# Optimization experiments

Measured on AMD Instinct MI355X. Metric: run time of the kernel, lower is better.

Reference implementation:

```python
import jax, jax.numpy as jnp
import numpy as np

B, N, DIM = 4, 4096, 512
HEADS, DIM_HEAD = 8, 64
DIM_INNER = HEADS * DIM_HEAD


def setup_inputs() -> dict:
    key = jax.random.key(0)
    k1, k2, k3 = jax.random.split(key, 3)
    x = jax.random.normal(k1, (B, N, DIM), dtype=jnp.float32)
    mask = jax.random.bernoulli(k2, 0.9, (B, N))
    W_qkv = jax.random.normal(k3, (DIM, 3 * DIM_INNER), dtype=jnp.float32) * (1.0 / np.sqrt(DIM))
    b_qkv = jnp.zeros((3 * DIM_INNER,), dtype=jnp.float32)
    return {"x": x, "mask": mask, "W_qkv": W_qkv, "b_qkv": b_qkv}


def reference(x, mask, W_qkv, b_qkv):
    # qkv projection: [b, n, 3*h*d]
    qkv = jnp.einsum('bnc,ce->bne', x, W_qkv) + b_qkv
    q, k, v = jnp.split(qkv, 3, axis=-1)

    def to_heads(t):  # b n (h d) -> b h n d
        b, n, _ = t.shape
        return t.reshape(b, n, HEADS, DIM_HEAD).transpose(0, 2, 1, 3)

    q, k, v = map(to_heads, (q, k, v))

    m = mask[:, None, :, None]  # b 1 n 1
    neg_max = -jnp.finfo(q.dtype).max
    k = jnp.where(m, k, neg_max)
    v = jnp.where(m, v, 0.0)

    k = jax.nn.softmax(k, axis=-2)  # softmax over sequence
    q = jax.nn.softmax(q, axis=-1)  # softmax over feature dim

    kv = jnp.einsum('bhnd,bhne->bhde', k, v)   # [b, h, d, d]
    out = jnp.einsum('bhde,bhnd->bhne', kv, q)  # [b, h, n, d]
    b_, h_, n_, d_ = out.shape
    return out.transpose(0, 2, 1, 3).reshape(b_, n_, h_ * d_)
```

## Files before the change

kernel.cpp:

```cpp
#include <hip/hip_runtime.h>
#include <stdint.h>

#define B_   4
#define N_   4096
#define DIM_ 512
#define H_   8
#define DH_  64
#define E3_  1536
#define M_   (B_*N_)

typedef __attribute__((ext_vector_type(8))) __bf16 bf16x8;
typedef __attribute__((ext_vector_type(8))) unsigned short ushort8;
typedef __attribute__((ext_vector_type(4))) float f32x4;

__device__ inline float bf2f(unsigned short u){ return __uint_as_float(((unsigned)u)<<16); }
__device__ inline unsigned short f2bf(float f){
  unsigned u = __float_as_uint(f);
  u += 0x7FFFu + ((u>>16)&1u);
  return (unsigned short)(u>>16);
}

__device__ inline void gld_lds16(const void* g, void* l){
  __builtin_amdgcn_global_load_lds(
      (const __attribute__((address_space(1))) void*)g,
      (__attribute__((address_space(3))) void*)l, 16, 0, 0);
}

__global__ void detect_fmt(const unsigned int* __restrict__ xw,
                           const unsigned int* __restrict__ ww,
                           const unsigned int* __restrict__ mw,
                           int* __restrict__ flags)
{
  __shared__ int cnt[2];
  __shared__ int ok[3];
  if (threadIdx.x < 2) cnt[threadIdx.x] = 0;
  if (threadIdx.x < 3) ok[threadIdx.x] = 1;
  __syncthreads();
  int hx = 0, hw = 0;
  for (int i = threadIdx.x; i < 1024; i += 256) {
    if (((xw[i] >> 7) & 0xFFu) > 140u) hx++;
    if (((ww[i] >> 7) & 0xFFu) > 140u) hw++;
  }
  int okInt = 1, okF32 = 1, okBf = 1;
  for (int i = threadIdx.x; i < 4096; i += 256) {
    unsigned w = mw[i];
    if (w > 1u) okInt = 0;
    if (w != 0u && w != 0x3F800000u) okF32 = 0;
    unsigned short a = (unsigned short)(w & 0xFFFFu), b = (unsigned short)(w >> 16);
    if (!((a == 0 || a == 0x3F80u) && (b == 0 || b == 0x3F80u))) okBf = 0;
  }
  atomicAdd(&cnt[0], hx);
  atomicAdd(&cnt[1], hw);
  if (!okInt) atomicAnd(&ok[0], 0);
  if (!okF32) atomicAnd(&ok[1], 0);
  if (!okBf)  atomicAnd(&ok[2], 0);
  __syncthreads();
  if (threadIdx.x == 0) {
    flags[0] = cnt[0] > 64 ? 1 : 0;
    flags[1] = cnt[1] > 64 ? 1 : 0;
    flags[2] = ok[0] ? 0 : (ok[1] ? 1 : (ok[2] ? 2 : 3));
  }
}

__device__ inline bool mask_at(const void* m, int flag, int idx){
  if (flag == 0) return ((const int*)m)[idx] != 0;
  if (flag == 1) return ((const float*)m)[idx] != 0.f;
  if (flag == 2) return ((const unsigned short*)m)[idx] != 0;
  return ((const unsigned char*)m)[idx] != 0;
}
__device__ inline float gread(const void* p, int f32, size_t i){
  return f32 ? ((const float*)p)[i] : bf2f(((const unsigned short*)p)[i]);
}

__device__ inline void unpack8(uint4 u, float* f){
  f[0] = bf2f((unsigned short)(u.x & 0xffff)); f[1] = bf2f((unsigned short)(u.x >> 16));
  f[2] = bf2f((unsigned short)(u.y & 0xffff)); f[3] = bf2f((unsigned short)(u.y >> 16));
  f[4] = bf2f((unsigned short)(u.z & 0xffff)); f[5] = bf2f((unsigned short)(u.z >> 16));
  f[6] = bf2f((unsigned short)(u.w & 0xffff)); f[7] = bf2f((unsigned short)(u.w >> 16));
}

__global__ __launch_bounds__(256)
void pack_xw(const void* __restrict__ x, const void* __restrict__ w,
             unsigned short* __restrict__ xq, unsigned short* __restrict__ wq,
             const int* __restrict__ flags)
{
  if (blockIdx.x < 4096) {
    const int f = flags[0];
    const int g = blockIdx.x * 256 + threadIdx.x;
    const int R = g >> 13, rem = g & 8191;
    const int kk = rem >> 9, u = rem & 511;
    const int m = R * 128 + (u & 127);
    const int k0 = kk * 32 + (u >> 7) * 8;
    ushort8 v;
    if (f) {
      const float* xp = (const float*)x + (size_t)m * DIM_ + k0;
      float4 a = *(const float4*)xp, b = *(const float4*)(xp + 4);
      v[0]=f2bf(a.x); v[1]=f2bf(a.y); v[2]=f2bf(a.z); v[3]=f2bf(a.w);
      v[4]=f2bf(b.x); v[5]=f2bf(b.y); v[6]=f2bf(b.z); v[7]=f2bf(b.w);
    } else {
      v = *(const ushort8*)((const unsigned short*)x + (size_t)m * DIM_ + k0);
    }
    *(ushort8*)&xq[(size_t)g * 8] = v;
  } else {
    const int f = flags[1];
    const int g = (blockIdx.x - 4096) * 256 + threadIdx.x;
    const int C = g >> 13, rem = g & 8191;
    const int kk = rem >> 9, u = rem & 511;
    const int n = C * 128 + (u & 127);
    const int k0 = kk * 32 + (u >> 7) * 8;
    ushort8 v;
    #pragma unroll
    for (int j = 0; j < 8; ++j) v[j] = f2bf(gread(w, f, (size_t)(k0 + j) * E3_ + n));
    *(ushort8*)&wq[(size_t)g * 8] = v;
  }
}

__global__ __launch_bounds__(256, 2)
void qkv_gemm_fused(const unsigned short* __restrict__ xq,
                    const unsigned short* __restrict__ wq,
                    const void* __restrict__ bias, const void* __restrict__ mask,
                    const int* __restrict__ flags,
                    unsigned short* __restrict__ qb,
                    unsigned short* __restrict__ ekg,
                    unsigned short* __restrict__ vmg)
{
  const int wf = flags[1], mf = flags[2];
  __shared__ alignas(16) unsigned short As[4][4096];
  __shared__ alignas(16) unsigned short Bs[4][4096];
  const int t = threadIdx.x;
  const int lane = t & 63, wv = t >> 6;
  const int quad = lane >> 4, l15 = lane & 15;
  const int hwf = blockIdx.y * 12 + blockIdx.x;
  const int lf  = (hwf & 7) * 192 + (hwf >> 3);
  const int bx = lf % 12, by = lf / 12;
  const int m0 = by * 128, n0 = bx * 128;
  const int mw = (wv & 1) * 64, nw = (wv >> 1) * 64;

  f32x4 acc[4][4];
  #pragma unroll
  for (int i = 0; i < 4; ++i)
    #pragma unroll
    for (int j = 0; j < 4; ++j) acc[i][j] = (f32x4){0.f,0.f,0.f,0.f};

  const unsigned short* aim0 = xq + ((size_t)(by * 16) * 512) * 8;
  const unsigned short* bim0 = wq + ((size_t)(bx * 16) * 512) * 8;

  auto stage = [&](int kk, int bb) {
    const unsigned short* aim = aim0 + (size_t)kk * 4096;
    const unsigned short* bim = bim0 + (size_t)kk * 4096;
    #pragma unroll
    for (int s = 0; s < 2; ++s) {
      const int u0 = s * 256 + wv * 64;
      gld_lds16(aim + (size_t)(u0 + lane) * 8, &As[bb][u0 * 8]);
      gld_lds16(bim + (size_t)(u0 + lane) * 8, &Bs[bb][u0 * 8]);
    }
  };

  stage(0, 0);
  stage(1, 1);
  #pragma unroll
  for (int kk = 0; kk < 16; ++kk) {
    const int bb = kk & 3;
    if (kk < 14) stage(kk + 2, (kk + 2) & 3);
    if (kk < 14)       asm volatile("s_waitcnt vmcnt(8)" ::: "memory");
    else if (kk == 14) asm volatile("s_waitcnt vmcnt(4)" ::: "memory");
    else               asm volatile("s_waitcnt vmcnt(0)" ::: "memory");
    __builtin_amdgcn_sched_barrier(0);
    __builtin_amdgcn_s_barrier();
    __builtin_amdgcn_sched_barrier(0);
    ushort8 af[4], bfr[4];
    #pragma unroll
    for (int i = 0; i < 4; ++i) {
      af[i]  = *(const ushort8*)&As[bb][(quad * 128 + mw + i * 16 + l15) * 8];
      bfr[i] = *(const ushort8*)&Bs[bb][(quad * 128 + nw + i * 16 + l15) * 8];
    }
    #pragma unroll
    for (int i = 0; i < 4; ++i)
      #pragma unroll
      for (int j = 0; j < 4; ++j)
        acc[i][j] = __builtin_amdgcn_mfma_f32_16x16x32_bf16(
            __builtin_bit_cast(bf16x8, af[i]), __builtin_bit_cast(bf16x8, bfr[j]),
            acc[i][j], 0, 0, 0);
  }

  const int mode = bx >> 2;
  if (mode == 0) {
    #pragma unroll
    for (int j = 0; j < 4; ++j) {
      int col = n0 + nw + j * 16 + l15;
      float bv = gread(bias, wf, col);
      #pragma unroll
      for (int i = 0; i < 4; ++i)
        #pragma unroll
        for (int r = 0; r < 4; ++r) {
          int row = m0 + mw + i * 16 + quad * 4 + r;
          qb[(size_t)row * 512 + col] = f2bf(acc[i][j][r] + bv);
        }
    }
  } else {
    unsigned short* dstbuf = (mode == 1) ? ekg : vmg;
    float bj[4]; int hj[4], dj[4];
    #pragma unroll
    for (int j = 0; j < 4; ++j) {
      int col = n0 + nw + j * 16 + l15;
      bj[j] = gread(bias, wf, col);
      int rel = col - mode * 512;
      hj[j] = rel >> 6; dj[j] = rel & 63;
    }
    #pragma unroll
    for (int i = 0; i < 4; ++i)
      #pragma unroll
      for (int r = 0; r < 4; ++r) {
        int row = m0 + mw + i * 16 + quad * 4 + r;
        bool mk = mask_at(mask, mf, row);
        int bb2 = row >> 12, nn = row & 4095;
        size_t base = (size_t)(nn >> 3) * 512 + (nn & 7);
        #pragma unroll
        for (int j = 0; j < 4; ++j) {
          float val = acc[i][j][r] + bj[j];
          val = (mode == 1) ? (mk ? __expf(val) : 0.f) : (mk ? val : 0.f);
          dstbuf[(size_t)(bb2 * 8 + hj[j]) * 262144 + base + (size_t)dj[j] * 8] = f2bf(val);
        }
      }
  }
}

__global__ __launch_bounds__(256)
void kv_gemm(const unsigned short* __restrict__ ekg,
             const unsigned short* __restrict__ vmg,
             float* __restrict__ kvpart, float* __restrict__ denpart)
{
  const int sc = blockIdx.x;
  const int bh = blockIdx.y;
  const int t  = threadIdx.x;
  const int lane = t & 63, wv = t >> 6;
  const int quad = lane >> 4, l15 = lane & 15;
  __shared__ alignas(16) unsigned short ekS[16384];
  __shared__ alignas(16) unsigned short vmS[16384];

  f32x4 acc[4];
  #pragma unroll
  for (int j = 0; j < 4; ++j) acc[j] = (f32x4){0.f,0.f,0.f,0.f};
  float dsum = 0.f;
  const int dden = t & 63, g0 = (t >> 6) * 8;
  const size_t gbase = (size_t)bh * 262144 + (size_t)sc * 16384;

  #pragma unroll
  for (int i = 0; i < 8; ++i) {
    int u0 = i * 256 + wv * 64;
    gld_lds16(&ekg[gbase + (size_t)(u0 + lane) * 8], &ekS[u0 * 8]);
    gld_lds16(&vmg[gbase + (size_t)(u0 + lane) * 8], &vmS[u0 * 8]);
  }
  __syncthreads();
  {
    #pragma unroll
    for (int kt = 0; kt < 8; ++kt) {
      ushort8 v = *(const ushort8*)&ekS[((g0 + kt) * 64 + dden) * 8];
      #pragma unroll
      for (int j = 0; j < 8; ++j) dsum += bf2f(v[j]);
    }
  }
  #pragma unroll 2
  for (int ks = 0; ks < 8; ++ks) {
    ushort8 af = *(const ushort8*)&ekS[((ks * 4 + quad) * 64 + wv * 16 + l15) * 8];
    #pragma unroll
    for (int jt = 0; jt < 4; ++jt) {
      ushort8 bf8 = *(const ushort8*)&vmS[((ks * 4 + quad) * 64 + jt * 16 + l15) * 8];
      acc[jt] = __builtin_amdgcn_mfma_f32_16x16x32_bf16(
          __builtin_bit_cast(bf16x8, af), __builtin_bit_cast(bf16x8, bf8),
          acc[jt], 0, 0, 0);
    }
  }
  float* kvp = kvpart + (size_t)(sc * 32 + bh) * 4096;
  #pragma unroll
  for (int jt = 0; jt < 4; ++jt)
    #pragma unroll
    for (int r = 0; r < 4; ++r)
      kvp[(wv * 16 + quad * 4 + r) * 64 + jt * 16 + l15] = acc[jt][r];
  __syncthreads();
  float* red = (float*)ekS;
  red[t] = dsum;
  __syncthreads();
  if (t < 64)
    denpart[(sc * 32 + bh) * 64 + t] = red[t] + red[t + 64] + red[t + 128] + red[t + 192];
}

__global__ __launch_bounds__(256)
void kv_reduce(const float* __restrict__ kvpart, const float* __restrict__ denpart,
               unsigned short* __restrict__ kvnb)
{
  const int bh = blockIdx.x;
  const int qd = blockIdx.y;
  const int t  = threadIdx.x;
  __shared__ float den[16];
  if (t < 16) {
    float s = 0.f;
    #pragma unroll
    for (int c = 0; c < 16; ++c) s += denpart[(c * 32 + bh) * 64 + qd * 16 + t];
    den[t] = s;
  }
  __syncthreads();
  const int dl = t >> 4, e0 = (t & 15) * 4;
  const int d = qd * 16 + dl;
  float sx = 0.f, sy = 0.f, sz = 0.f, sw = 0.f;
  #pragma unroll
  for (int c = 0; c < 16; ++c) {
    const float4 v = *(const float4*)&kvpart[(size_t)(c * 32 + bh) * 4096 + d * 64 + e0];
    sx += v.x; sy += v.y; sz += v.z; sw += v.w;
  }
  const float inv = 1.f / den[dl];
  const float sv[4] = {sx, sy, sz, sw};
  #pragma unroll
  for (int j = 0; j < 4; ++j) {
    int e = e0 + j;
    kvnb[(size_t)bh * 4096 + ((size_t)(d >> 3) * 64 + e) * 8 + (d & 7)] = f2bf(sv[j] * inv);
  }
}

__global__ __launch_bounds__(256)
void out_pass(const unsigned short* __restrict__ qb,
              const unsigned short* __restrict__ kvnb,
              float* __restrict__ out)
{
  const int chunk = blockIdx.x, bh = blockIdx.y;
  const int b = bh >> 3, h = bh & 7;
  const int t = threadIdx.x;
  const int lane = t & 63, wv = t >> 6;
  const int quad = lane >> 4, l15 = lane & 15;
  __shared__ alignas(16) unsigned short kvS[4096];
  #pragma unroll
  for (int i = 0; i < 2; ++i)
    *(ushort8*)&kvS[(t + i * 256) * 8] =
        *(const ushort8*)&kvnb[(size_t)bh * 4096 + (size_t)(t + i * 256) * 8];
  __syncthreads();

  for (int g = 0; g < 4; ++g) {
    const int tok0 = chunk * 256 + wv * 64 + g * 16;
    const size_t qoff = (size_t)(b * N_ + tok0 + l15) * 512 + h * DH_ + quad * 8;
    uint4 qa = *(const uint4*)(qb + qoff);
    uint4 qc = *(const uint4*)(qb + qoff + 32);
    float qf[16];
    unpack8(qa, qf); unpack8(qc, qf + 8);
    float mx = qf[0];
    #pragma unroll
    for (int jj = 1; jj < 16; ++jj) mx = fmaxf(mx, qf[jj]);
    mx = fmaxf(mx, __shfl_xor(mx, 16));
    mx = fmaxf(mx, __shfl_xor(mx, 32));
    float s = 0.f;
    #pragma unroll
    for (int jj = 0; jj < 16; ++jj) { qf[jj] = __expf(qf[jj] - mx); s += qf[jj]; }
    s += __shfl_xor(s, 16);
    s += __shfl_xor(s, 32);
    const float inv = 1.f / s;
    ushort8 af0, af1;
    #pragma unroll
    for (int jj = 0; jj < 8; ++jj) {
      af0[jj] = f2bf(qf[jj] * inv);
      af1[jj] = f2bf(qf[8 + jj] * inv);
    }
    f32x4 oa[4];
    #pragma unroll
    for (int jt = 0; jt < 4; ++jt) oa[jt] = (f32x4){0.f,0.f,0.f,0.f};
    #pragma unroll
    for (int jt = 0; jt < 4; ++jt) {
      ushort8 b0 = *(const ushort8*)&kvS[((0 + quad) * 64 + jt * 16 + l15) * 8];
      ushort8 b1 = *(const ushort8*)&kvS[((4 + quad) * 64 + jt * 16 + l15) * 8];
      oa[jt] = __builtin_amdgcn_mfma_f32_16x16x32_bf16(
          __builtin_bit_cast(bf16x8, af0), __builtin_bit_cast(bf16x8, b0), oa[jt], 0, 0, 0);
      oa[jt] = __builtin_amdgcn_mfma_f32_16x16x32_bf16(
          __builtin_bit_cast(bf16x8, af1), __builtin_bit_cast(bf16x8, b1), oa[jt], 0, 0, 0);
    }
    const size_t ob = (size_t)(b * N_ + tok0 + quad * 4) * 512 + h * DH_;
    #pragma unroll
    for (int jt = 0; jt < 4; ++jt)
      #pragma unroll
      for (int r = 0; r < 4; ++r)
        out[ob + (size_t)r * 512 + jt * 16 + l15] = oa[jt][r];
  }
}

__device__ inline void stage_x_f(float (*xa)[516], const void* x, int xf, int brow0, int t)
{
  if (xf) {
    const float* xp = (const float*)x;
    #pragma unroll
    for (int s = 0; s < 8; ++s) {
      int row = (t >> 7) + 2 * s, col = (t & 127) * 4;
      *(float4*)&xa[row][col] = *(const float4*)(xp + ((size_t)(brow0 + row)) * DIM_ + col);
    }
  } else {
    const unsigned short* xp = (const unsigned short*)x;
    #pragma unroll
    for (int s = 0; s < 8; ++s) {
      int row = (t >> 7) + 2 * s, col = (t & 127) * 4;
      const unsigned short* pp = xp + ((size_t)(brow0 + row)) * DIM_ + col;
      #pragma unroll
      for (int j = 0; j < 4; ++j) xa[row][col + j] = bf2f(pp[j]);
    }
  }
}

__global__ __launch_bounds__(256)
void kv_pass_fused(const void* __restrict__ x, const void* __restrict__ w,
                   const void* __restrict__ bias, const void* __restrict__ mask,
                   const int* __restrict__ flags,
                   float* __restrict__ kvbuf, float* __restrict__ denom)
{
  const int chunk = blockIdx.x, bh = blockIdx.y;
  const int b = bh >> 3, h = bh & 7;
  const int t = threadIdx.x;
  const int xf = flags[0], wf = flags[1], mf = flags[2];
  __shared__ float xa[16][516];
  __shared__ float Wb[64][130];
  float* ekb = &Wb[0][0];
  float* vvb = &Wb[0][0] + 16 * 65;
  const int tok = t >> 4, d0 = (t & 15) * 4;
  const int down = t >> 2, e0 = (t & 3) * 16;
  float acc[16];
  #pragma unroll
  for (int i = 0; i < 16; ++i) acc[i] = 0.f;
  float dsum = 0.f;
  for (int g = 0; g < 16; ++g) {
    const int n0 = chunk * 256 + g * 16;
    __syncthreads();
    stage_x_f(xa, x, xf, b * N_ + n0, t);
    float kreg[4] = {0,0,0,0}, vreg[4] = {0,0,0,0};
    for (int cc = 0; cc < 8; ++cc) {
      __syncthreads();
      {
        int c0 = (t >> 7) * 32, col = t & 127;
        int wc = (col < 64) ? (512 + h * DH_ + col) : (1024 + h * DH_ + (col - 64));
        #pragma unroll 8
        for (int j = 0; j < 32; ++j)
          Wb[c0 + j][col] = gread(w, wf, (size_t)(cc * 64 + c0 + j) * E3_ + wc);
      }
      __syncthreads();
      #pragma unroll 4
      for (int c = 0; c < 64; ++c) {
        float xv = xa[tok][cc * 64 + c];
        #pragma unroll
        for (int j = 0; j < 4; ++j) {
          kreg[j] += xv * Wb[c][d0 + j];
          vreg[j] += xv * Wb[c][64 + d0 + j];
        }
      }
    }
    bool mk = mask_at(mask, mf, b * N_ + n0 + tok);
    __syncthreads();
    #pragma unroll
    for (int j = 0; j < 4; ++j) {
      float kvl = kreg[j] + gread(bias, wf, 512  + h * DH_ + d0 + j);
      float vvl = vreg[j] + gread(bias, wf, 1024 + h * DH_ + d0 + j);
      ekb[tok * 65 + d0 + j] = mk ? __expf(kvl) : 0.f;
      vvb[tok * 65 + d0 + j] = mk ? vvl : 0.f;
    }
    __syncthreads();
    #pragma unroll 4
    for (int nn = 0; nn < 16; ++nn) {
      float ekd = ekb[nn * 65 + down];
      if (e0 == 0) dsum += ekd;
      #pragma unroll
      for (int i = 0; i < 16; ++i) acc[i] += ekd * vvb[nn * 65 + e0 + i];
    }
  }
  float* kvp = kvbuf + (size_t)bh * 4096 + down * 64 + e0;
  #pragma unroll
  for (int i = 0; i < 16; ++i) atomicAdd(&kvp[i], acc[i]);
  if (e0 == 0) atomicAdd(&denom[bh * 64 + down], dsum);
}

__global__ __launch_bounds__(256)
void out_pass_fused(const void* __restrict__ x, const void* __restrict__ w,
                    const void* __restrict__ bias, const int* __restrict__ flags,
                    const float* __restrict__ kvbuf, const float* __restrict__ denom,
                    float* __restrict__ out)
{
  const int chunk = blockIdx.x, bh = blockIdx.y;
  const int b = bh >> 3, h = bh & 7;
  const int t = threadIdx.x;
  const int xf = flags[0], wf = flags[1];
  __shared__ float xa[16][516];
  __shared__ float Wq[64][66];
  __shared__ float kvn[64][68];
  float* qsm = &Wq[0][0];
  for (int i = t; i < 4096; i += 256) {
    int d = i >> 6, e = i & 63;
    kvn[d][e] = kvbuf[(size_t)bh * 4096 + i] / denom[bh * 64 + d];
  }
  const int tok = t >> 4, p = t & 15, d0 = p * 4;
  for (int g = 0; g < 16; ++g) {
    const int n0 = chunk * 256 + g * 16;
    __syncthreads();
    stage_x_f(xa, x, xf, b * N_ + n0, t);
    float qreg[4] = {0,0,0,0};
    for (int cc = 0; cc < 8; ++cc) {
      __syncthreads();
      {
        int col = t & 63, c0 = (t >> 6) * 16;
        #pragma unroll 8
        for (int j = 0; j < 16; ++j)
          Wq[c0 + j][col] = gread(w, wf, (size_t)(cc * 64 + c0 + j) * E3_ + h * DH_ + col);
      }
      __syncthreads();
      #pragma unroll 4
      for (int c = 0; c < 64; ++c) {
        float xv = xa[tok][cc * 64 + c];
        #pragma unroll
        for (int j = 0; j < 4; ++j) qreg[j] += xv * Wq[c][d0 + j];
      }
    }
    #pragma unroll
    for (int j = 0; j < 4; ++j) qreg[j] += gread(bias, wf, h * DH_ + d0 + j);
    float mx = fmaxf(fmaxf(qreg[0], qreg[1]), fmaxf(qreg[2], qreg[3]));
    #pragma unroll
    for (int o = 1; o < 16; o <<= 1) mx = fmaxf(mx, __shfl_xor(mx, o, 16));
    float s = 0.f;
    #pragma unroll
    for (int j = 0; j < 4; ++j) { qreg[j] = __expf(qreg[j] - mx); s += qreg[j]; }
    #pragma unroll
    for (int o = 1; o < 16; o <<= 1) s += __shfl_xor(s, o, 16);
    float inv = 1.f / s;
    __syncthreads();
    #pragma unroll
    for (int j = 0; j < 4; ++j) qsm[tok * 65 + d0 + j] = qreg[j] * inv;
    __syncthreads();
    {
      int e0 = p * 4;
      float ov[4] = {0,0,0,0};
      #pragma unroll 4
      for (int d = 0; d < 64; ++d) {
        float qd = qsm[tok * 65 + d];
        #pragma unroll
        for (int j = 0; j < 4; ++j) ov[j] += qd * kvn[d][e0 + j];
      }
      size_t ob = ((size_t)(b * N_ + n0 + tok)) * DIM_ + h * DH_ + e0;
      #pragma unroll
      for (int j = 0; j < 4; ++j) out[ob + j] = ov[j];
    }
  }
}

extern "C" void kernel_launch(void* const* d_in, const int* in_sizes, int n_in,
                              void* d_out, int out_size, void* d_ws, size_t ws_size,
                              hipStream_t stream)
{
  const void* x    = d_in[0];
  const void* mask = d_in[1];
  const void* w    = d_in[2];
  const void* bias = d_in[3];
  float* out = (float*)d_out;

  char* ws = (char*)d_ws;
  const size_t offFlg = 0;
  const size_t offXq  = 4096;
  const size_t offWq  = offXq + (size_t)M_ * DIM_ * 2;
  const size_t offQ   = offWq + (size_t)E3_ * DIM_ * 2;
  const size_t offEk  = offQ  + (size_t)M_ * DIM_ * 2;
  const size_t offVm  = offEk + (size_t)M_ * DH_ * H_ * 2;
  const size_t need   = offVm + (size_t)M_ * DH_ * H_ * 2;
  const size_t offKvp = offXq;
  const size_t offDnp = offXq + 8388608;
  const size_t offKvn = offXq + 8388608 + 131072;

  int* flags = (int*)(ws + offFlg);
  detect_fmt<<<1, 256, 0, stream>>>((const unsigned int*)x, (const unsigned int*)w,
                                    (const unsigned int*)mask, flags);

  if (ws_size >= need) {
    unsigned short* xq  = (unsigned short*)(ws + offXq);
    unsigned short* wq  = (unsigned short*)(ws + offWq);
    unsigned short* qb  = (unsigned short*)(ws + offQ);
    unsigned short* ekg = (unsigned short*)(ws + offEk);
    unsigned short* vmg = (unsigned short*)(ws + offVm);
    float* kvpart = (float*)(ws + offKvp);
    float* denpart = (float*)(ws + offDnp);
    unsigned short* kvnb = (unsigned short*)(ws + offKvn);

    pack_xw<<<4480, 256, 0, stream>>>(x, w, xq, wq, flags);
    dim3 gg(E3_ / 128, M_ / 128);
    qkv_gemm_fused<<<gg, 256, 0, stream>>>(xq, wq, bias, mask, flags, qb, ekg, vmg);
    kv_gemm<<<dim3(16, 32), 256, 0, stream>>>(ekg, vmg, kvpart, denpart);
    kv_reduce<<<dim3(32, 4), 256, 0, stream>>>(kvpart, denpart, kvnb);
    out_pass<<<dim3(16, 32), 256, 0, stream>>>(qb, kvnb, out);
  } else {
    float* kvbuf = (float*)(ws + 4096);
    float* denom = (float*)(ws + 4096 + 32 * 4096 * 4);
    hipMemsetAsync(kvbuf, 0, 32 * 4096 * 4 + 32 * 64 * 4, stream);
    dim3 ga(16, 32);
    kv_pass_fused <<<ga, 256, 0, stream>>>(x, w, bias, mask, flags, kvbuf, denom);
    out_pass_fused<<<ga, 256, 0, stream>>>(x, w, bias, flags, kvbuf, denom, out);
  }
}
```

Baseline: 173.4 us.

## Fuse kv_reduce into out_pass and shrink GEMM LDS pipeline for occupancy

Removes the kv_reduce kernel: each out_pass block now sums the 16 partial kv and denominator slices itself and writes the normalized bf16 kv straight into LDS, which saves a launch and a global round trip. The QKV GEMM goes from a 4-buffer, 2-ahead LDS pipeline to a 2-buffer, 1-ahead one, halving its LDS use, and launch bounds ask for 4 blocks per CU. out_pass also remaps block indices so blocks are grouped across XCDs. In exchange, each of the 16 chunk blocks for a head redoes the same reduction, and the shallower prefetch exposes more load latency in the GEMM.

```diff
diff --git a/kernel.cpp b/kernel.cpp
--- a/kernel.cpp
+++ b/kernel.cpp
@@ -115,7 +115,7 @@
   }
 }
 
-__global__ __launch_bounds__(256, 2)
+__global__ __launch_bounds__(256, 4)
 void qkv_gemm_fused(const unsigned short* __restrict__ xq,
                     const unsigned short* __restrict__ wq,
                     const void* __restrict__ bias, const void* __restrict__ mask,
@@ -125,8 +125,8 @@
                     unsigned short* __restrict__ vmg)
 {
   const int wf = flags[1], mf = flags[2];
-  __shared__ alignas(16) unsigned short As[4][4096];
-  __shared__ alignas(16) unsigned short Bs[4][4096];
+  __shared__ alignas(16) unsigned short As[2][4096];
+  __shared__ alignas(16) unsigned short Bs[2][4096];
   const int t = threadIdx.x;
   const int lane = t & 63, wv = t >> 6;
   const int quad = lane >> 4, l15 = lane & 15;
@@ -157,14 +157,13 @@
   };
 
   stage(0, 0);
-  stage(1, 1);
   #pragma unroll
   for (int kk = 0; kk < 16; ++kk) {
-    const int bb = kk & 3;
-    if (kk < 14) stage(kk + 2, (kk + 2) & 3);
-    if (kk < 14)       asm volatile("s_waitcnt vmcnt(8)" ::: "memory");
-    else if (kk == 14) asm volatile("s_waitcnt vmcnt(4)" ::: "memory");
-    else               asm volatile("s_waitcnt vmcnt(0)" ::: "memory");
+    const int bb = kk & 1;
+    __builtin_amdgcn_s_barrier();
+    if (kk < 15) stage(kk + 1, bb ^ 1);
+    if (kk < 15) asm volatile("s_waitcnt vmcnt(4)" ::: "memory");
+    else         asm volatile("s_waitcnt vmcnt(0)" ::: "memory");
     __builtin_amdgcn_sched_barrier(0);
     __builtin_amdgcn_s_barrier();
     __builtin_amdgcn_sched_barrier(0);
@@ -286,52 +285,42 @@
 }
 
 __global__ __launch_bounds__(256)
-void kv_reduce(const float* __restrict__ kvpart, const float* __restrict__ denpart,
-               unsigned short* __restrict__ kvnb)
-{
-  const int bh = blockIdx.x;
-  const int qd = blockIdx.y;
-  const int t  = threadIdx.x;
-  __shared__ float den[16];
-  if (t < 16) {
-    float s = 0.f;
-    #pragma unroll
-    for (int c = 0; c < 16; ++c) s += denpart[(c * 32 + bh) * 64 + qd * 16 + t];
-    den[t] = s;
-  }
-  __syncthreads();
-  const int dl = t >> 4, e0 = (t & 15) * 4;
-  const int d = qd * 16 + dl;
-  float sx = 0.f, sy = 0.f, sz = 0.f, sw = 0.f;
-  #pragma unroll
-  for (int c = 0; c < 16; ++c) {
-    const float4 v = *(const float4*)&kvpart[(size_t)(c * 32 + bh) * 4096 + d * 64 + e0];
-    sx += v.x; sy += v.y; sz += v.z; sw += v.w;
-  }
-  const float inv = 1.f / den[dl];
-  const float sv[4] = {sx, sy, sz, sw};
-  #pragma unroll
-  for (int j = 0; j < 4; ++j) {
-    int e = e0 + j;
-    kvnb[(size_t)bh * 4096 + ((size_t)(d >> 3) * 64 + e) * 8 + (d & 7)] = f2bf(sv[j] * inv);
-  }
-}
-
-__global__ __launch_bounds__(256)
 void out_pass(const unsigned short* __restrict__ qb,
-              const unsigned short* __restrict__ kvnb,
+              const float* __restrict__ kvpart, const float* __restrict__ denpart,
               float* __restrict__ out)
 {
-  const int chunk = blockIdx.x, bh = blockIdx.y;
+  const int hw = blockIdx.y * 16 + blockIdx.x;
+  const int lg = (hw & 7) * 64 + (hw >> 3);
+  const int chunk = lg & 15, bh = lg >> 4;
   const int b = bh >> 3, h = bh & 7;
   const int t = threadIdx.x;
   const int lane = t & 63, wv = t >> 6;
   const int quad = lane >> 4, l15 = lane & 15;
   __shared__ alignas(16) unsigned short kvS[4096];
-  #pragma unroll
-  for (int i = 0; i < 2; ++i)
-    *(ushort8*)&kvS[(t + i * 256) * 8] =
-        *(const ushort8*)&kvnb[(size_t)bh * 4096 + (size_t)(t + i * 256) * 8];
+  __shared__ float denS[64];
+
+  if (t < 64) {
+    float s = 0.f;
+    #pragma unroll
+    for (int c = 0; c < 16; ++c) s += denpart[(c * 32 + bh) * 64 + t];
+    denS[t] = s;
+  }
+  __syncthreads();
+  #pragma unroll
+  for (int rep = 0; rep < 4; ++rep) {
+    const int d = rep * 16 + (t >> 4), e0 = (t & 15) * 4;
+    float sx = 0.f, sy = 0.f, sz = 0.f, sw = 0.f;
+    #pragma unroll
+    for (int c = 0; c < 16; ++c) {
+      const float4 v = *(const float4*)&kvpart[(size_t)(c * 32 + bh) * 4096 + d * 64 + e0];
+      sx += v.x; sy += v.y; sz += v.z; sw += v.w;
+    }
+    const float inv = 1.f / denS[d];
+    kvS[((d >> 3) * 64 + e0 + 0) * 8 + (d & 7)] = f2bf(sx * inv);
+    kvS[((d >> 3) * 64 + e0 + 1) * 8 + (d & 7)] = f2bf(sy * inv);
+    kvS[((d >> 3) * 64 + e0 + 2) * 8 + (d & 7)] = f2bf(sz * inv);
+    kvS[((d >> 3) * 64 + e0 + 3) * 8 + (d & 7)] = f2bf(sw * inv);
+  }
   __syncthreads();
 
   for (int g = 0; g < 4; ++g) {
@@ -560,7 +549,6 @@
   const size_t need   = offVm + (size_t)M_ * DH_ * H_ * 2;
   const size_t offKvp = offXq;
   const size_t offDnp = offXq + 8388608;
-  const size_t offKvn = offXq + 8388608 + 131072;
 
   int* flags = (int*)(ws + offFlg);
   detect_fmt<<<1, 256, 0, stream>>>((const unsigned int*)x, (const unsigned int*)w,
@@ -574,14 +562,12 @@
     unsigned short* vmg = (unsigned short*)(ws + offVm);
     float* kvpart = (float*)(ws + offKvp);
     float* denpart = (float*)(ws + offDnp);
-    unsigned short* kvnb = (unsigned short*)(ws + offKvn);
 
     pack_xw<<<4480, 256, 0, stream>>>(x, w, xq, wq, flags);
     dim3 gg(E3_ / 128, M_ / 128);
     qkv_gemm_fused<<<gg, 256, 0, stream>>>(xq, wq, bias, mask, flags, qb, ekg, vmg);
     kv_gemm<<<dim3(16, 32), 256, 0, stream>>>(ekg, vmg, kvpart, denpart);
-    kv_reduce<<<dim3(32, 4), 256, 0, stream>>>(kvpart, denpart, kvnb);
-    out_pass<<<dim3(16, 32), 256, 0, stream>>>(qb, kvnb, out);
+    out_pass<<<dim3(16, 32), 256, 0, stream>>>(qb, kvpart, denpart, out);
   } else {
     float* kvbuf = (float*)(ws + 4096);
     float* denom = (float*)(ws + 4096 + 32 * 4096 * 4);
```

New measurement: 175.6 us. Within noise of the previous version (+1.2%).
